# Performance work log

Hardware: AMD Instinct MI355X
Metric: run time of the kernel (lower is better)

## Reference

```python
import jax, jax.numpy as jnp
import numpy as np

N_NODES = 50000


def gcn_conv(x, W, b, src, dst, ew, n):
    """PyG-style GCNConv: D^-1/2 (A+I) D^-1/2 X W + b with self-loops of weight 1."""
    h = x @ W                                   # [N, out]
    loop = jnp.arange(n, dtype=src.dtype)
    s = jnp.concatenate([src, loop])            # [E+N]
    d = jnp.concatenate([dst, loop])
    w = jnp.concatenate([ew, jnp.ones((n,), dtype=x.dtype)])
    deg = jax.ops.segment_sum(w, d, num_segments=n)
    dinv = jnp.where(deg > 0, jax.lax.rsqrt(deg), 0.0)
    norm = dinv[s] * w * dinv[d]                # [E+N]
    out = jax.ops.segment_sum(h[s] * norm[:, None], d, num_segments=n)
    return out + b


def setup_inputs() -> dict:
    key = jax.random.key(0)
    ks = jax.random.split(key, 12)
    in_feats, hidden = 128, 128
    half = hidden // 2
    E = 800000
    x = jax.random.normal(ks[0], (N_NODES, in_feats), dtype=jnp.float32)
    edge_index = jax.random.randint(ks[1], (2, E), 0, N_NODES, dtype=jnp.int64)
    edge_weight = jax.random.uniform(ks[2], (E,), dtype=jnp.float32)
    def lin(k, fan_in, shape):
        bound = 1.0 / np.sqrt(fan_in)
        return jax.random.uniform(k, shape, minval=-bound, maxval=bound, dtype=jnp.float32)
    return {
        "x": x,
        "edge_index": edge_index,
        "edge_weight": edge_weight,
        "W1": lin(ks[3], in_feats, (in_feats, hidden)),
        "b1": jnp.zeros((hidden,), jnp.float32),
        "W2": lin(ks[4], hidden, (hidden, hidden)),
        "b2": jnp.zeros((hidden,), jnp.float32),
        "Ws": lin(ks[5], in_feats, (in_feats, hidden)),
        "bs": lin(ks[6], in_feats, (hidden,)),
        "Wl": lin(ks[7], in_feats, (in_feats, half)),
        "bl": jnp.zeros((half,), jnp.float32),
        "Wl2": lin(ks[8], half, (half, 1)),
        "bl2": lin(ks[9], half, (1,)),
    }


def reference(x, edge_index, edge_weight, W1, b1, W2, b2, Ws, bs, Wl, bl, Wl2, bl2):
    n = x.shape[0]
    src, dst = edge_index[0], edge_index[1]
    # conv1 + ReLU over neighbors
    h_neighbors = jax.nn.relu(gcn_conv(x, W1, b1, src, dst, edge_weight, n))
    # leader score: GCNConv -> ReLU -> Linear(.,1) -> sigmoid, per node
    ls_h = jax.nn.relu(gcn_conv(x, Wl, bl, src, dst, edge_weight, n))
    leader_score = jax.nn.sigmoid(ls_h @ Wl2 + bl2)        # [N, 1]
    # gated fusion of self projection vs neighbor aggregation
    h_self_proj = x @ Ws + bs
    h_new = (1.0 - leader_score) * h_neighbors + leader_score * h_self_proj
    h_final = jax.nn.relu(gcn_conv(h_new, W2, b2, src, dst, edge_weight, n))
    return (h_final, leader_score)
```

## Files before the change

kernel.cpp:

```cpp
#include <hip/hip_runtime.h>
#include <math.h>

#define THREADS 256
#define ELLS 96
#define GEMM_YSTRIDE 104
#define NPHA 256
#define BSHIFT 7
#define NBMAX 392
#define BCAP 4096
#define PMAX 5872
#define LMAX 736

typedef unsigned int uint32;
typedef unsigned long long ull64;
typedef __attribute__((ext_vector_type(8))) short bf16x8;
typedef __attribute__((ext_vector_type(4))) float f32x4;
typedef __attribute__((ext_vector_type(2))) float f32x2;

__device__ __forceinline__ unsigned short f2bf_rne(float x) {
  uint32 u = __float_as_uint(x);
  u += 0x7fffu + ((u >> 16) & 1u);
  return (unsigned short)(u >> 16);
}

__device__ __forceinline__ f32x2 dw2f2(uint32 d) {
  f32x2 r;
  r.x = __uint_as_float(d << 16);
  r.y = __uint_as_float(d & 0xffff0000u);
  return r;
}


__global__ __launch_bounds__(256) void prep_fused(uint32* __restrict__ gcnt, int n,
                                                  const float* __restrict__ W1, const float* __restrict__ Wl,
                                                  const float* __restrict__ Ws, const float* __restrict__ W2,
                                                  unsigned short* __restrict__ whi, unsigned short* __restrict__ wlo,
                                                  const float* __restrict__ x, unsigned short* __restrict__ xraw,
                                                  int nW) {
  int b = blockIdx.x;
  int t = threadIdx.x;
  if (b == 0) {
    for (int k = t; k < NBMAX; k += 256) gcnt[k] = 0u;
  }
  if (b < 1 + nW) {
    if (b == 0) return;
    int idx = (b - 1) * 256 + t;
    if (idx >= 448 * 128) return;
    int slot = idx >> 7;
    int k = idx & 127;
    const float* W; int ncol, ncols;
    if (slot < 128)      { W = W1; ncol = slot;       ncols = 128; }
    else if (slot < 192) { W = Wl; ncol = slot - 128; ncols = 64;  }
    else if (slot < 320) { W = Ws; ncol = slot - 192; ncols = 128; }
    else                 { W = W2; ncol = slot - 320; ncols = 128; }
    float v = W[(size_t)k * ncols + ncol];
    unsigned short hi = f2bf_rne(v);
    float hif = __uint_as_float((uint32)hi << 16);
    unsigned short lo = f2bf_rne(v - hif);
    whi[idx] = hi;
    wlo[idx] = lo;
  } else {
    int i = (b - 1 - nW) * 256 + t;
    if (i >= n * 16) return;
    const float* px = x + (size_t)i * 8;
    float4 a = *(const float4*)px;
    float4 c = *(const float4*)(px + 4);
    ushort4 r0, r1;
    r0.x = f2bf_rne(a.x); r0.y = f2bf_rne(a.y); r0.z = f2bf_rne(a.z); r0.w = f2bf_rne(a.w);
    r1.x = f2bf_rne(c.x); r1.y = f2bf_rne(c.y); r1.z = f2bf_rne(c.z); r1.w = f2bf_rne(c.w);
    *(ushort4*)(xraw + (size_t)i * 8) = r0;
    *(ushort4*)(xraw + (size_t)i * 8 + 4) = r1;
  }
}


struct Chunk {
  const unsigned short* A;
  const unsigned short* whi;
  const unsigned short* wlo;
  const float* bias;
  void* out;
  int ostride;
  int obf16;
};
struct GemmArgs { Chunk c[2]; };

__device__ __forceinline__ void gemm_body(const Chunk& d, int M, int nTiles, int tile0, int tstride) {
  const unsigned short* A = d.A;
  int w = threadIdx.x >> 6, lane = threadIdx.x & 63;
  int n16 = lane & 15, quad = lane >> 4;

  bf16x8 Bh[4][4], Bl[4][4];
  {
    const unsigned short* wh = d.whi + (size_t)n16 * 128 + quad * 8;
    const unsigned short* wl = d.wlo + (size_t)n16 * 128 + quad * 8;
#pragma unroll
    for (int ct = 0; ct < 4; ct++)
#pragma unroll
      for (int ks = 0; ks < 4; ks++) {
        Bh[ct][ks] = *(const bf16x8*)(wh + ct * 16 * 128 + ks * 32);
        Bl[ct][ks] = *(const bf16x8*)(wl + ct * 16 * 128 + ks * 32);
      }
  }
  float bv[4];
#pragma unroll
  for (int ct = 0; ct < 4; ct++) bv[ct] = d.bias ? d.bias[ct * 16 + n16] : 0.f;

  int tile = tile0;
  bf16x8 av0[4], av1[4];
  if (tile < nTiles) {
    int bm = tile * 128;
    int r0 = bm + w * 32 + n16, r1 = r0 + 16;
    int r0c = r0 < M ? r0 : M - 1;
    int r1c = r1 < M ? r1 : M - 1;
    const unsigned short* a0 = A + (size_t)r0c * 128 + quad * 8;
    const unsigned short* a1 = A + (size_t)r1c * 128 + quad * 8;
#pragma unroll
    for (int ks = 0; ks < 4; ks++) {
      av0[ks] = *(const bf16x8*)(a0 + ks * 32);
      av1[ks] = *(const bf16x8*)(a1 + ks * 32);
    }
  }

  for (; tile < nTiles; tile += tstride) {
    int nxt = tile + tstride;
    bf16x8 nv0[4], nv1[4];
    if (nxt < nTiles) {
      int bm = nxt * 128;
      int r0 = bm + w * 32 + n16, r1 = r0 + 16;
      int r0c = r0 < M ? r0 : M - 1;
      int r1c = r1 < M ? r1 : M - 1;
      const unsigned short* a0 = A + (size_t)r0c * 128 + quad * 8;
      const unsigned short* a1 = A + (size_t)r1c * 128 + quad * 8;
#pragma unroll
      for (int ks = 0; ks < 4; ks++) {
        nv0[ks] = *(const bf16x8*)(a0 + ks * 32);
        nv1[ks] = *(const bf16x8*)(a1 + ks * 32);
      }
    }

    f32x4 acc[2][4];
#pragma unroll
    for (int rt = 0; rt < 2; rt++)
#pragma unroll
      for (int ct = 0; ct < 4; ct++) acc[rt][ct] = (f32x4){0.f, 0.f, 0.f, 0.f};

#pragma unroll
    for (int ks = 0; ks < 4; ks++)
#pragma unroll
      for (int ct = 0; ct < 4; ct++) {
        acc[0][ct] = __builtin_amdgcn_mfma_f32_16x16x32_bf16(av0[ks], Bh[ct][ks], acc[0][ct], 0, 0, 0);
        acc[0][ct] = __builtin_amdgcn_mfma_f32_16x16x32_bf16(av0[ks], Bl[ct][ks], acc[0][ct], 0, 0, 0);
        acc[1][ct] = __builtin_amdgcn_mfma_f32_16x16x32_bf16(av1[ks], Bh[ct][ks], acc[1][ct], 0, 0, 0);
        acc[1][ct] = __builtin_amdgcn_mfma_f32_16x16x32_bf16(av1[ks], Bl[ct][ks], acc[1][ct], 0, 0, 0);
      }

    int bm = tile * 128;
#pragma unroll
    for (int ct = 0; ct < 4; ct++) {
      int col = ct * 16 + n16;
#pragma unroll
      for (int rt = 0; rt < 2; rt++) {
#pragma unroll
        for (int reg = 0; reg < 4; reg++) {
          int row = bm + w * 32 + rt * 16 + quad * 4 + reg;
          if (row < M) {
            float v = acc[rt][ct][reg] + bv[ct];
            if (d.obf16)
              ((unsigned short*)d.out)[(size_t)row * d.ostride + col] = f2bf_rne(v);
            else
              ((float*)d.out)[(size_t)row * d.ostride + col] = v;
          }
        }
      }
    }

#pragma unroll
    for (int ks = 0; ks < 4; ks++) { av0[ks] = nv0[ks]; av1[ks] = nv1[ks]; }
  }
}


__global__ __launch_bounds__(256, 2) void fused_sg(GemmArgs args, int M, int nTiles, int nGemm,
                                                   const int* __restrict__ ei, const float* __restrict__ ew,
                                                   uint32* __restrict__ gcnt, uint2* __restrict__ staging, int E) {
  __shared__ uint32 cntS[NBMAX], offS[NBMAX], gbS[NBMAX], curS[NBMAX];
  __shared__ unsigned short lineBk[LMAX];
  __shared__ uint2 sortedS[PMAX];
  __shared__ uint32 Ptot;

  int b = blockIdx.x;
  int gemmIdx = -1, phIdx = -1;
  int twice = nGemm * 2;
  if (b < twice) {
    if (b & 1) gemmIdx = b >> 1; else phIdx = b >> 1;
  } else {
    phIdx = nGemm + (b - twice);
  }

  if (phIdx >= 0) {
    int t = threadIdx.x;
    int per = (E + NPHA - 1) / NPHA;
    int start = phIdx * per;
    int end = start + per; if (end > E) end = E;
    for (int k = t; k < NBMAX; k += 256) cntS[k] = 0u;
    __syncthreads();
    for (int i = start + t; i < end; i += 256)
      atomicAdd(&cntS[(uint32)ei[E + i] >> BSHIFT], 1u);
    __syncthreads();
    if (t < 64) {
      uint32 carry = 0;
      for (int base = 0; base < NBMAX; base += 64) {
        int k = base + t;
        uint32 v = (k < NBMAX) ? ((cntS[k] + 7u) & ~7u) : 0u;
        uint32 s = v;
#pragma unroll
        for (int dd = 1; dd < 64; dd <<= 1) {
          uint32 o = __shfl_up(s, dd);
          if (t >= dd) s += o;
        }
        if (k < NBMAX) offS[k] = carry + s - v;
        carry += __shfl(s, 63);
      }
      if (t == 0) Ptot = carry;
    }
    __syncthreads();
    uint32 P = Ptot;
    for (int k = t; k < NBMAX; k += 256) {
      uint32 pc = (cntS[k] + 7u) & ~7u;
      gbS[k] = pc ? atomicAdd(&gcnt[k], pc) : 0u;
      curS[k] = 0u;
      uint32 l1 = (offS[k] + pc) >> 3;
      for (uint32 l = offS[k] >> 3; l < l1; l++) lineBk[l] = (unsigned short)k;
    }
    for (uint32 j = t; j < P; j += 256) sortedS[j] = make_uint2(0xFFFFFFFFu, 0u);
    __syncthreads();
    for (int i = start + t; i < end; i += 256) {
      int d = ei[E + i];
      int s = ei[i];
      float w = ew[i];
      int bk = d >> BSHIFT;
      uint32 pos = offS[bk] + atomicAdd(&curS[bk], 1u);
      sortedS[pos] = make_uint2(((uint32)(d & 127) << 24) | (uint32)s, __float_as_uint(w));
    }
    __syncthreads();
    for (uint32 j = t; j < P; j += 256) {
      int k = lineBk[j >> 3];
      uint32 idx = gbS[k] + (j - offS[k]);
      if (idx < BCAP)
        staging[(size_t)k * BCAP + idx] = sortedS[j];
    }
    return;
  }

  int chunkId = gemmIdx & 1;
  int ytile = gemmIdx >> 1;
  gemm_body(args.c[chunkId], M, nTiles, ytile, GEMM_YSTRIDE);
}


__global__ __launch_bounds__(256) void phaseB_kernel(const uint2* __restrict__ staging,
                                                     const uint32* __restrict__ gcnt,
                                                     int2* __restrict__ ell,
                                                     float* __restrict__ dinv, int* __restrict__ cnt32, int n) {
  __shared__ uint32 cntL[128], sumL[128];
  int b = blockIdx.x;
  int t = threadIdx.x;
  if (t < 128) { cntL[t] = 0u; sumL[t] = 0u; }
  __syncthreads();
  uint32 cnt = gcnt[b]; if (cnt > BCAP) cnt = BCAP;
  const uint2* sb = staging + (size_t)b * BCAP;
  int dbase = b << BSHIFT;
  for (uint32 i = t; i < cnt; i += 256) {
    uint2 en = sb[i];
    if ((en.x >> 24) == 0xFFu) continue;
    int dl = (int)(en.x >> 24);
    int s = (int)(en.x & 0xffffffu);
    float w = __uint_as_float(en.y);
    uint32 fx = (uint32)(w * 8388608.0f + 0.5f);
    atomicAdd(&sumL[dl], fx);
    uint32 slot = atomicAdd(&cntL[dl], 1u);
    if (slot < ELLS)
      ell[(size_t)(dbase + dl) * ELLS + slot] = make_int2(s, __float_as_int(w));
  }
  __syncthreads();
  if (t < 128) {
    int d = dbase + t;
    if (d < n) {
      const float S = 1.1920928955078125e-7f;
      dinv[d] = rsqrtf(1.0f + (float)sumL[t] * S);
      uint32 c = cntL[t];
      cnt32[d] = (int)(c < ELLS ? c : ELLS);
    }
  }
}


__global__ __launch_bounds__(256) void aggx_kernel(const unsigned short* __restrict__ xr,
                                                   const int* __restrict__ cnt,
                                                   const int2* __restrict__ csr,
                                                   const float* __restrict__ dinv,
                                                   unsigned short* __restrict__ z, int nnodes) {
  int wave = threadIdx.x >> 6;
  int lane = threadIdx.x & 63;
  int node = blockIdx.x * 4 + wave;
  if (node >= nnodes) return;
  int g = lane >> 4, q = lane & 15;
  int rs = node * ELLS;
  int n = cnt[node];
  float di = dinv[node];
  f32x2 dv2 = {di, di};

  f32x2 acc[4] = {};
  if (g == 0) {
    uint4 v = *(const uint4*)(xr + (size_t)node * 128 + 8 * q);
    acc[0] = dv2 * dw2f2(v.x); acc[1] = dv2 * dw2f2(v.y);
    acc[2] = dv2 * dw2f2(v.z); acc[3] = dv2 * dw2f2(v.w);
  }
  int e = g;
  for (; e + 4 < n; e += 8) {
    int2 en0 = csr[rs + e];
    int2 en1 = csr[rs + e + 4];
    float wz0 = __int_as_float(en0.y) * dinv[en0.x];
    float wz1 = __int_as_float(en1.y) * dinv[en1.x];
    f32x2 w0 = {wz0, wz0};
    f32x2 w1 = {wz1, wz1};
    uint4 a0 = *(const uint4*)(xr + (size_t)en0.x * 128 + 8 * q);
    uint4 a1 = *(const uint4*)(xr + (size_t)en1.x * 128 + 8 * q);
    acc[0] += w0 * dw2f2(a0.x) + w1 * dw2f2(a1.x);
    acc[1] += w0 * dw2f2(a0.y) + w1 * dw2f2(a1.y);
    acc[2] += w0 * dw2f2(a0.z) + w1 * dw2f2(a1.z);
    acc[3] += w0 * dw2f2(a0.w) + w1 * dw2f2(a1.w);
  }
  if (e < n) {
    int2 en = csr[rs + e];
    float wz0 = __int_as_float(en.y) * dinv[en.x];
    f32x2 w0 = {wz0, wz0};
    uint4 a0 = *(const uint4*)(xr + (size_t)en.x * 128 + 8 * q);
    acc[0] += w0 * dw2f2(a0.x);
    acc[1] += w0 * dw2f2(a0.y);
    acc[2] += w0 * dw2f2(a0.z);
    acc[3] += w0 * dw2f2(a0.w);
  }
#pragma unroll
  for (int k = 0; k < 4; k++) {
    acc[k].x += __shfl_xor(acc[k].x, 16);
    acc[k].y += __shfl_xor(acc[k].y, 16);
    acc[k].x += __shfl_xor(acc[k].x, 32);
    acc[k].y += __shfl_xor(acc[k].y, 32);
  }
  if (g == 0) {
    float r[8];
    r[0] = di * acc[0].x; r[1] = di * acc[0].y; r[2] = di * acc[1].x; r[3] = di * acc[1].y;
    r[4] = di * acc[2].x; r[5] = di * acc[2].y; r[6] = di * acc[3].x; r[7] = di * acc[3].y;
    ushort4 p0, p1;
    p0.x = f2bf_rne(r[0]); p0.y = f2bf_rne(r[1]); p0.z = f2bf_rne(r[2]); p0.w = f2bf_rne(r[3]);
    p1.x = f2bf_rne(r[4]); p1.y = f2bf_rne(r[5]); p1.z = f2bf_rne(r[6]); p1.w = f2bf_rne(r[7]);
    *(ushort4*)(z + (size_t)node * 128 + 8 * q) = p0;
    *(ushort4*)(z + (size_t)node * 128 + 8 * q + 4) = p1;
  }
}


__global__ __launch_bounds__(256) void gemm_fused(const unsigned short* __restrict__ z,
                                                  const unsigned short* __restrict__ hsp,
                                                  const unsigned short* __restrict__ whi,
                                                  const unsigned short* __restrict__ wlo,
                                                  const float* __restrict__ b1, const float* __restrict__ bl,
                                                  const float* __restrict__ Wl2, const float* __restrict__ bl2,
                                                  const float* __restrict__ dinv,
                                                  unsigned short* __restrict__ h2_out,
                                                  float* __restrict__ leader_out, int n) {
  __shared__ unsigned short hn[128][136];
  int tile = blockIdx.x;
  int w = threadIdx.x >> 6, lane = threadIdx.x & 63;
  int n16 = lane & 15, quad = lane >> 4;
  int bm = tile * 128;

  bf16x8 av[2][4];
#pragma unroll
  for (int rt = 0; rt < 2; rt++) {
    int r = bm + w * 32 + rt * 16 + n16;
    int rc = r < n ? r : n - 1;
    const unsigned short* a = z + (size_t)rc * 128 + quad * 8;
#pragma unroll
    for (int ks = 0; ks < 4; ks++) av[rt][ks] = *(const bf16x8*)(a + ks * 32);
  }

  float lgate[2][4];
  {
    f32x4 ls[2][4];
#pragma unroll
    for (int rt = 0; rt < 2; rt++)
#pragma unroll
      for (int cf = 0; cf < 4; cf++) ls[rt][cf] = (f32x4){0.f, 0.f, 0.f, 0.f};
#pragma unroll
    for (int cf = 0; cf < 4; cf++) {
      const unsigned short* wh = whi + (size_t)(128 + cf * 16 + n16) * 128 + quad * 8;
      const unsigned short* wl = wlo + (size_t)(128 + cf * 16 + n16) * 128 + quad * 8;
#pragma unroll
      for (int ks = 0; ks < 4; ks++) {
        bf16x8 Bh = *(const bf16x8*)(wh + ks * 32);
        bf16x8 Bl = *(const bf16x8*)(wl + ks * 32);
        ls[0][cf] = __builtin_amdgcn_mfma_f32_16x16x32_bf16(av[0][ks], Bh, ls[0][cf], 0, 0, 0);
        ls[0][cf] = __builtin_amdgcn_mfma_f32_16x16x32_bf16(av[0][ks], Bl, ls[0][cf], 0, 0, 0);
        ls[1][cf] = __builtin_amdgcn_mfma_f32_16x16x32_bf16(av[1][ks], Bh, ls[1][cf], 0, 0, 0);
        ls[1][cf] = __builtin_amdgcn_mfma_f32_16x16x32_bf16(av[1][ks], Bl, ls[1][cf], 0, 0, 0);
      }
    }
#pragma unroll
    for (int rt = 0; rt < 2; rt++)
#pragma unroll
      for (int reg = 0; reg < 4; reg++) {
        float p = 0.f;
#pragma unroll
        for (int cf = 0; cf < 4; cf++) {
          int col = cf * 16 + n16;
          p += fmaxf(ls[rt][cf][reg] + bl[col], 0.f) * Wl2[col];
        }
        p += __shfl_xor(p, 1);
        p += __shfl_xor(p, 2);
        p += __shfl_xor(p, 4);
        p += __shfl_xor(p, 8);
        float lv = 1.f / (1.f + expf(-(p + bl2[0])));
        lgate[rt][reg] = lv;
        int row = bm + w * 32 + rt * 16 + quad * 4 + reg;
        if (n16 == 0 && row < n) leader_out[row] = lv;
      }
  }

  float dirr[2][4];
#pragma unroll
  for (int rt = 0; rt < 2; rt++)
#pragma unroll
    for (int reg = 0; reg < 4; reg++) {
      int row = bm + w * 32 + rt * 16 + quad * 4 + reg;
      dirr[rt][reg] = row < n ? dinv[row] : 0.f;
    }

#pragma unroll
  for (int cf = 0; cf < 8; cf++) {
    f32x4 h0 = {0.f, 0.f, 0.f, 0.f}, h1v = {0.f, 0.f, 0.f, 0.f};
    const unsigned short* wh = whi + (size_t)(cf * 16 + n16) * 128 + quad * 8;
    const unsigned short* wl = wlo + (size_t)(cf * 16 + n16) * 128 + quad * 8;
#pragma unroll
    for (int ks = 0; ks < 4; ks++) {
      bf16x8 Bh = *(const bf16x8*)(wh + ks * 32);
      bf16x8 Bl = *(const bf16x8*)(wl + ks * 32);
      h0 = __builtin_amdgcn_mfma_f32_16x16x32_bf16(av[0][ks], Bh, h0, 0, 0, 0);
      h0 = __builtin_amdgcn_mfma_f32_16x16x32_bf16(av[0][ks], Bl, h0, 0, 0, 0);
      h1v = __builtin_amdgcn_mfma_f32_16x16x32_bf16(av[1][ks], Bh, h1v, 0, 0, 0);
      h1v = __builtin_amdgcn_mfma_f32_16x16x32_bf16(av[1][ks], Bl, h1v, 0, 0, 0);
    }
    int col = cf * 16 + n16;
    float bc = b1[col];
#pragma unroll
    for (int rt = 0; rt < 2; rt++) {
      f32x4 a = rt ? h1v : h0;
#pragma unroll
      for (int reg = 0; reg < 4; reg++) {
        int row = bm + w * 32 + rt * 16 + quad * 4 + reg;
        int rc = row < n ? row : n - 1;
        float hs = __uint_as_float((uint32)hsp[(size_t)rc * 128 + col] << 16);
        float rl = fmaxf(a[reg] + bc, 0.f);
        float lv = lgate[rt][reg];
        float hv = ((1.f - lv) * rl + lv * hs) * dirr[rt][reg];
        hn[w * 32 + rt * 16 + quad * 4 + reg][col] = f2bf_rne(hv);
      }
    }
  }
  __syncthreads();

  bf16x8 av2[2][4];
#pragma unroll
  for (int rt = 0; rt < 2; rt++)
#pragma unroll
    for (int ks = 0; ks < 4; ks++)
      av2[rt][ks] = *(const bf16x8*)&hn[w * 32 + rt * 16 + n16][quad * 8 + ks * 32];
#pragma unroll
  for (int cf = 0; cf < 8; cf++) {
    f32x4 h0 = {0.f, 0.f, 0.f, 0.f}, h1v = {0.f, 0.f, 0.f, 0.f};
    const unsigned short* wh = whi + (size_t)(320 + cf * 16 + n16) * 128 + quad * 8;
    const unsigned short* wl = wlo + (size_t)(320 + cf * 16 + n16) * 128 + quad * 8;
#pragma unroll
    for (int ks = 0; ks < 4; ks++) {
      bf16x8 Bh = *(const bf16x8*)(wh + ks * 32);
      bf16x8 Bl = *(const bf16x8*)(wl + ks * 32);
      h0 = __builtin_amdgcn_mfma_f32_16x16x32_bf16(av2[0][ks], Bh, h0, 0, 0, 0);
      h0 = __builtin_amdgcn_mfma_f32_16x16x32_bf16(av2[0][ks], Bl, h0, 0, 0, 0);
      h1v = __builtin_amdgcn_mfma_f32_16x16x32_bf16(av2[1][ks], Bh, h1v, 0, 0, 0);
      h1v = __builtin_amdgcn_mfma_f32_16x16x32_bf16(av2[1][ks], Bl, h1v, 0, 0, 0);
    }
    int col = cf * 16 + n16;
#pragma unroll
    for (int rt = 0; rt < 2; rt++) {
      f32x4 a = rt ? h1v : h0;
#pragma unroll
      for (int reg = 0; reg < 4; reg++) {
        int row = bm + w * 32 + rt * 16 + quad * 4 + reg;
        if (row < n) h2_out[(size_t)row * 128 + col] = f2bf_rne(a[reg]);
      }
    }
  }
}


__global__ __launch_bounds__(256) void agg_conv2_kernel(const unsigned short* __restrict__ h,
                                                        const int* __restrict__ cnt,
                                                        const int2* __restrict__ csr,
                                                        const float* __restrict__ dinv, const float* __restrict__ bias,
                                                        float* __restrict__ out, int nnodes) {
  int wave = threadIdx.x >> 6;
  int lane = threadIdx.x & 63;
  int node = blockIdx.x * 4 + wave;
  if (node >= nnodes) return;
  int g = lane >> 4;
  int q = lane & 15;
  int rs = node * ELLS;
  int n = cnt[node];
  float di = dinv[node];

  f32x2 acc[4] = {};
  if (g == 0) {
    uint4 v = *(const uint4*)(h + (size_t)node * 128 + 8 * q);
    acc[0] = dw2f2(v.x); acc[1] = dw2f2(v.y);
    acc[2] = dw2f2(v.z); acc[3] = dw2f2(v.w);
  }
  int e = g;
  for (; e + 4 < n; e += 8) {
    int2 en0 = csr[rs + e];
    int2 en1 = csr[rs + e + 4];
    f32x2 w0 = {__int_as_float(en0.y), __int_as_float(en0.y)};
    f32x2 w1 = {__int_as_float(en1.y), __int_as_float(en1.y)};
    uint4 v0 = *(const uint4*)(h + (size_t)en0.x * 128 + 8 * q);
    uint4 v1 = *(const uint4*)(h + (size_t)en1.x * 128 + 8 * q);
    acc[0] += w0 * dw2f2(v0.x) + w1 * dw2f2(v1.x);
    acc[1] += w0 * dw2f2(v0.y) + w1 * dw2f2(v1.y);
    acc[2] += w0 * dw2f2(v0.z) + w1 * dw2f2(v1.z);
    acc[3] += w0 * dw2f2(v0.w) + w1 * dw2f2(v1.w);
  }
  if (e < n) {
    int2 en = csr[rs + e];
    f32x2 w0 = {__int_as_float(en.y), __int_as_float(en.y)};
    uint4 v = *(const uint4*)(h + (size_t)en.x * 128 + 8 * q);
    acc[0] += w0 * dw2f2(v.x);
    acc[1] += w0 * dw2f2(v.y);
    acc[2] += w0 * dw2f2(v.z);
    acc[3] += w0 * dw2f2(v.w);
  }
#pragma unroll
  for (int k = 0; k < 4; k++) {
    acc[k].x += __shfl_xor(acc[k].x, 16);
    acc[k].y += __shfl_xor(acc[k].y, 16);
    acc[k].x += __shfl_xor(acc[k].x, 32);
    acc[k].y += __shfl_xor(acc[k].y, 32);
  }
  if (g == 0) {
    float b[8], r[8];
    *(float4*)&b[0] = *(const float4*)(bias + 8 * q);
    *(float4*)&b[4] = *(const float4*)(bias + 8 * q + 4);
    float a[8];
    a[0] = acc[0].x; a[1] = acc[0].y; a[2] = acc[1].x; a[3] = acc[1].y;
    a[4] = acc[2].x; a[5] = acc[2].y; a[6] = acc[3].x; a[7] = acc[3].y;
#pragma unroll
    for (int j = 0; j < 8; j++) r[j] = fmaxf(di * a[j] + b[j], 0.f);
    *(float4*)(out + (size_t)node * 128 + 8 * q) = *(float4*)&r[0];
    *(float4*)(out + (size_t)node * 128 + 8 * q + 4) = *(float4*)&r[4];
  }
}


extern "C" void kernel_launch(void* const* d_in, const int* in_sizes, int n_in,
                              void* d_out, int out_size, void* d_ws, size_t ws_size,
                              hipStream_t stream) {
  const float* x   = (const float*)d_in[0];
  const int*   ei  = (const int*)d_in[1];
  const float* ew  = (const float*)d_in[2];
  const float* W1  = (const float*)d_in[3];
  const float* b1  = (const float*)d_in[4];
  const float* W2  = (const float*)d_in[5];
  const float* b2  = (const float*)d_in[6];
  const float* Wsp = (const float*)d_in[7];
  const float* bs  = (const float*)d_in[8];
  const float* Wl  = (const float*)d_in[9];
  const float* bl  = (const float*)d_in[10];
  const float* Wl2 = (const float*)d_in[11];
  const float* bl2 = (const float*)d_in[12];

  const int N = in_sizes[0] / 128;
  const int E = in_sizes[1] / 2;
  const int NB = (N + 127) >> BSHIFT;

  char* ws = (char*)d_ws;
  size_t off = 0;
  auto alloc = [&](size_t bytes) -> void* {
    void* p = ws + off;
    off = (off + bytes + 255) & ~(size_t)255;
    return p;
  };
  uint32* gcnt     = (uint32*)alloc((size_t)NBMAX * 4);
  uint2* staging   = (uint2*)alloc((size_t)NBMAX * BCAP * 8);
  float* dinv      = (float*)alloc((size_t)N * 4);
  int*   cnt32     = (int*)alloc((size_t)N * 4);
  int2*  ell       = (int2*)alloc((size_t)N * ELLS * 8);
  unsigned short* xraw  = (unsigned short*)alloc((size_t)N * 128 * 2);
  unsigned short* zbf   = (unsigned short*)alloc((size_t)N * 128 * 2);
  unsigned short* h2bf  = (unsigned short*)alloc((size_t)N * 128 * 2);
  unsigned short* hspbf = (unsigned short*)alloc((size_t)N * 128 * 2);
  unsigned short* whi = (unsigned short*)alloc((size_t)448 * 128 * 2);
  unsigned short* wlo = (unsigned short*)alloc((size_t)448 * 128 * 2);

  float* h_final = (float*)d_out;
  float* leader  = (float*)d_out + (size_t)N * 128;

  int gWave = (N + 3) / 4;
  int nTiles = (N + 127) / 128;
  int nCast = (N * 16 + 255) / 256;
  int nW = (448 * 128 + 255) / 256;

  prep_fused<<<1 + nW + nCast, 256, 0, stream>>>(gcnt, N, W1, Wl, Wsp, W2, whi, wlo, x, xraw, nW);

  {
    GemmArgs ga;
    ga.c[0] = {xraw, whi + 192 * 128, wlo + 192 * 128, bs,      hspbf,      128, 1};
    ga.c[1] = {xraw, whi + 256 * 128, wlo + 256 * 128, bs + 64, hspbf + 64, 128, 1};
    int nGemm = 2 * GEMM_YSTRIDE;
    int totalBlocks = NPHA + nGemm;
    fused_sg<<<totalBlocks, 256, 0, stream>>>(ga, N, nTiles, nGemm, ei, ew, gcnt, staging, E);
  }

  phaseB_kernel<<<NB, 256, 0, stream>>>(staging, gcnt, ell, dinv, cnt32, N);

  aggx_kernel<<<gWave, 256, 0, stream>>>(xraw, cnt32, ell, dinv, zbf, N);

  gemm_fused<<<nTiles, 256, 0, stream>>>(zbf, hspbf, whi, wlo, b1, bl, Wl2, bl2,
                                         dinv, h2bf, leader, N);

  agg_conv2_kernel<<<gWave, 256, 0, stream>>>(h2bf, cnt32, ell,
                                              dinv, b2, h_final, N);
}
```

Before: 252.3 us.

## Shrink fused GEMM tile to 16 rows per wave, drop block barrier

The fused conv1/leader/conv2-transform GEMM kernel now gives each wave 16 rows instead of 32 and launches twice as many blocks (64 rows per block). Each wave keeps a private LDS slice, so the __syncthreads between the two GEMM stages goes away. The self-projection values are also preloaded up front. This aims to raise occupancy and parallelism across the GPU's CUs, at the cost of every wave loading the weight B fragments for half as many rows, which doubles weight traffic per row.

```diff
diff --git a/kernel.cpp b/kernel.cpp
--- a/kernel.cpp
+++ b/kernel.cpp
@@ -371,29 +371,38 @@
                                                   const float* __restrict__ dinv,
                                                   unsigned short* __restrict__ h2_out,
                                                   float* __restrict__ leader_out, int n) {
-  __shared__ unsigned short hn[128][136];
-  int tile = blockIdx.x;
-  int w = threadIdx.x >> 6, lane = threadIdx.x & 63;
+  __shared__ unsigned short hn[4][16][136];
+  int wave = threadIdx.x >> 6, lane = threadIdx.x & 63;
   int n16 = lane & 15, quad = lane >> 4;
-  int bm = tile * 128;
-
-  bf16x8 av[2][4];
-#pragma unroll
-  for (int rt = 0; rt < 2; rt++) {
-    int r = bm + w * 32 + rt * 16 + n16;
+  int base = blockIdx.x * 64 + wave * 16;
+  if (base >= n) return;
+
+  bf16x8 av[4];
+  {
+    int r = base + n16;
     int rc = r < n ? r : n - 1;
     const unsigned short* a = z + (size_t)rc * 128 + quad * 8;
 #pragma unroll
-    for (int ks = 0; ks < 4; ks++) av[rt][ks] = *(const bf16x8*)(a + ks * 32);
-  }
-
-  float lgate[2][4];
+    for (int ks = 0; ks < 4; ks++) av[ks] = *(const bf16x8*)(a + ks * 32);
+  }
+
+  float dirr[4];
+  unsigned short hsv[8][4];
+#pragma unroll
+  for (int reg = 0; reg < 4; reg++) {
+    int row = base + quad * 4 + reg;
+    dirr[reg] = row < n ? dinv[row] : 0.f;
+    int rc = row < n ? row : n - 1;
+#pragma unroll
+    for (int cf = 0; cf < 8; cf++)
+      hsv[cf][reg] = hsp[(size_t)rc * 128 + cf * 16 + n16];
+  }
+
+  float lgate[4];
   {
-    f32x4 ls[2][4];
-#pragma unroll
-    for (int rt = 0; rt < 2; rt++)
-#pragma unroll
-      for (int cf = 0; cf < 4; cf++) ls[rt][cf] = (f32x4){0.f, 0.f, 0.f, 0.f};
+    f32x4 ls[4];
+#pragma unroll
+    for (int cf = 0; cf < 4; cf++) ls[cf] = (f32x4){0.f, 0.f, 0.f, 0.f};
 #pragma unroll
     for (int cf = 0; cf < 4; cf++) {
       const unsigned short* wh = whi + (size_t)(128 + cf * 16 + n16) * 128 + quad * 8;
@@ -402,104 +411,74 @@
       for (int ks = 0; ks < 4; ks++) {
         bf16x8 Bh = *(const bf16x8*)(wh + ks * 32);
         bf16x8 Bl = *(const bf16x8*)(wl + ks * 32);
-        ls[0][cf] = __builtin_amdgcn_mfma_f32_16x16x32_bf16(av[0][ks], Bh, ls[0][cf], 0, 0, 0);
-        ls[0][cf] = __builtin_amdgcn_mfma_f32_16x16x32_bf16(av[0][ks], Bl, ls[0][cf], 0, 0, 0);
-        ls[1][cf] = __builtin_amdgcn_mfma_f32_16x16x32_bf16(av[1][ks], Bh, ls[1][cf], 0, 0, 0);
-        ls[1][cf] = __builtin_amdgcn_mfma_f32_16x16x32_bf16(av[1][ks], Bl, ls[1][cf], 0, 0, 0);
+        ls[cf] = __builtin_amdgcn_mfma_f32_16x16x32_bf16(av[ks], Bh, ls[cf], 0, 0, 0);
+        ls[cf] = __builtin_amdgcn_mfma_f32_16x16x32_bf16(av[ks], Bl, ls[cf], 0, 0, 0);
       }
     }
 #pragma unroll
-    for (int rt = 0; rt < 2; rt++)
-#pragma unroll
-      for (int reg = 0; reg < 4; reg++) {
-        float p = 0.f;
-#pragma unroll
-        for (int cf = 0; cf < 4; cf++) {
-          int col = cf * 16 + n16;
-          p += fmaxf(ls[rt][cf][reg] + bl[col], 0.f) * Wl2[col];
-        }
-        p += __shfl_xor(p, 1);
-        p += __shfl_xor(p, 2);
-        p += __shfl_xor(p, 4);
-        p += __shfl_xor(p, 8);
-        float lv = 1.f / (1.f + expf(-(p + bl2[0])));
-        lgate[rt][reg] = lv;
-        int row = bm + w * 32 + rt * 16 + quad * 4 + reg;
-        if (n16 == 0 && row < n) leader_out[row] = lv;
+    for (int reg = 0; reg < 4; reg++) {
+      float p = 0.f;
+#pragma unroll
+      for (int cf = 0; cf < 4; cf++) {
+        int col = cf * 16 + n16;
+        p += fmaxf(ls[cf][reg] + bl[col], 0.f) * Wl2[col];
       }
-  }
-
-  float dirr[2][4];
-#pragma unroll
-  for (int rt = 0; rt < 2; rt++)
-#pragma unroll
-    for (int reg = 0; reg < 4; reg++) {
-      int row = bm + w * 32 + rt * 16 + quad * 4 + reg;
-      dirr[rt][reg] = row < n ? dinv[row] : 0.f;
-    }
+      p += __shfl_xor(p, 1);
+      p += __shfl_xor(p, 2);
+      p += __shfl_xor(p, 4);
+      p += __shfl_xor(p, 8);
+      float lv = 1.f / (1.f + expf(-(p + bl2[0])));
+      lgate[reg] = lv;
+      int row = base + quad * 4 + reg;
+      if (n16 == 0 && row < n) leader_out[row] = lv;
+    }
+  }
 
 #pragma unroll
   for (int cf = 0; cf < 8; cf++) {
-    f32x4 h0 = {0.f, 0.f, 0.f, 0.f}, h1v = {0.f, 0.f, 0.f, 0.f};
+    f32x4 h0 = {0.f, 0.f, 0.f, 0.f};
     const unsigned short* wh = whi + (size_t)(cf * 16 + n16) * 128 + quad * 8;
     const unsigned short* wl = wlo + (size_t)(cf * 16 + n16) * 128 + quad * 8;
 #pragma unroll
     for (int ks = 0; ks < 4; ks++) {
       bf16x8 Bh = *(const bf16x8*)(wh + ks * 32);
       bf16x8 Bl = *(const bf16x8*)(wl + ks * 32);
-      h0 = __builtin_amdgcn_mfma_f32_16x16x32_bf16(av[0][ks], Bh, h0, 0, 0, 0);
-      h0 = __builtin_amdgcn_mfma_f32_16x16x32_bf16(av[0][ks], Bl, h0, 0, 0, 0);
-      h1v = __builtin_amdgcn_mfma_f32_16x16x32_bf16(av[1][ks], Bh, h1v, 0, 0, 0);
-      h1v = __builtin_amdgcn_mfma_f32_16x16x32_bf16(av[1][ks], Bl, h1v, 0, 0, 0);
+      h0 = __builtin_amdgcn_mfma_f32_16x16x32_bf16(av[ks], Bh, h0, 0, 0, 0);
+      h0 = __builtin_amdgcn_mfma_f32_16x16x32_bf16(av[ks], Bl, h0, 0, 0, 0);
     }
     int col = cf * 16 + n16;
     float bc = b1[col];
 #pragma unroll
-    for (int rt = 0; rt < 2; rt++) {
-      f32x4 a = rt ? h1v : h0;
-#pragma unroll
-      for (int reg = 0; reg < 4; reg++) {
-        int row = bm + w * 32 + rt * 16 + quad * 4 + reg;
-        int rc = row < n ? row : n - 1;
-        float hs = __uint_as_float((uint32)hsp[(size_t)rc * 128 + col] << 16);
-        float rl = fmaxf(a[reg] + bc, 0.f);
-        float lv = lgate[rt][reg];
-        float hv = ((1.f - lv) * rl + lv * hs) * dirr[rt][reg];
-        hn[w * 32 + rt * 16 + quad * 4 + reg][col] = f2bf_rne(hv);
-      }
-    }
-  }
-  __syncthreads();
-
-  bf16x8 av2[2][4];
-#pragma unroll
-  for (int rt = 0; rt < 2; rt++)
-#pragma unroll
-    for (int ks = 0; ks < 4; ks++)
-      av2[rt][ks] = *(const bf16x8*)&hn[w * 32 + rt * 16 + n16][quad * 8 + ks * 32];
+    for (int reg = 0; reg < 4; reg++) {
+      float hs = __uint_as_float((uint32)hsv[cf][reg] << 16);
+      float rl = fmaxf(h0[reg] + bc, 0.f);
+      float lv = lgate[reg];
+      float hv = ((1.f - lv) * rl + lv * hs) * dirr[reg];
+      hn[wave][quad * 4 + reg][col] = f2bf_rne(hv);
+    }
+  }
+
+  bf16x8 av2[4];
+#pragma unroll
+  for (int ks = 0; ks < 4; ks++)
+    av2[ks] = *(const bf16x8*)&hn[wave][n16][quad * 8 + ks * 32];
 #pragma unroll
   for (int cf = 0; cf < 8; cf++) {
-    f32x4 h0 = {0.f, 0.f, 0.f, 0.f}, h1v = {0.f, 0.f, 0.f, 0.f};
+    f32x4 h0 = {0.f, 0.f, 0.f, 0.f};
     const unsigned short* wh = whi + (size_t)(320 + cf * 16 + n16) * 128 + quad * 8;
     const unsigned short* wl = wlo + (size_t)(320 + cf * 16 + n16) * 128 + quad * 8;
 #pragma unroll
     for (int ks = 0; ks < 4; ks++) {
       bf16x8 Bh = *(const bf16x8*)(wh + ks * 32);
       bf16x8 Bl = *(const bf16x8*)(wl + ks * 32);
-      h0 = __builtin_amdgcn_mfma_f32_16x16x32_bf16(av2[0][ks], Bh, h0, 0, 0, 0);
-      h0 = __builtin_amdgcn_mfma_f32_16x16x32_bf16(av2[0][ks], Bl, h0, 0, 0, 0);
-      h1v = __builtin_amdgcn_mfma_f32_16x16x32_bf16(av2[1][ks], Bh, h1v, 0, 0, 0);
-      h1v = __builtin_amdgcn_mfma_f32_16x16x32_bf16(av2[1][ks], Bl, h1v, 0, 0, 0);
+      h0 = __builtin_amdgcn_mfma_f32_16x16x32_bf16(av2[ks], Bh, h0, 0, 0, 0);
+      h0 = __builtin_amdgcn_mfma_f32_16x16x32_bf16(av2[ks], Bl, h0, 0, 0, 0);
     }
     int col = cf * 16 + n16;
 #pragma unroll
-    for (int rt = 0; rt < 2; rt++) {
-      f32x4 a = rt ? h1v : h0;
-#pragma unroll
-      for (int reg = 0; reg < 4; reg++) {
-        int row = bm + w * 32 + rt * 16 + quad * 4 + reg;
-        if (row < n) h2_out[(size_t)row * 128 + col] = f2bf_rne(a[reg]);
-      }
+    for (int reg = 0; reg < 4; reg++) {
+      int row = base + quad * 4 + reg;
+      if (row < n) h2_out[(size_t)row * 128 + col] = f2bf_rne(h0[reg]);
     }
   }
 }
@@ -617,6 +596,7 @@
   int nTiles = (N + 127) / 128;
   int nCast = (N * 16 + 255) / 256;
   int nW = (448 * 128 + 255) / 256;
+  int gFuse = (N + 63) / 64;
 
   prep_fused<<<1 + nW + nCast, 256, 0, stream>>>(gcnt, N, W1, Wl, Wsp, W2, whi, wlo, x, xraw, nW);
 
@@ -633,8 +613,8 @@
 
   aggx_kernel<<<gWave, 256, 0, stream>>>(xraw, cnt32, ell, dinv, zbf, N);
 
-  gemm_fused<<<nTiles, 256, 0, stream>>>(zbf, hspbf, whi, wlo, b1, bl, Wl2, bl2,
-                                         dinv, h2bf, leader, N);
+  gemm_fused<<<gFuse, 256, 0, stream>>>(zbf, hspbf, whi, wlo, b1, bl, Wl2, bl2,
+                                        dinv, h2bf, leader, N);
 
   agg_conv2_kernel<<<gWave, 256, 0, stream>>>(h2bf, cnt32, ell,
                                               dinv, b2, h_final, N);
```

Result: slower. 278.7 us (+10.5%).

## Make fused GEMM single-wave per block with prefetched weight fragments

Applied to the files above, without the earlier changes.

Turns the fused GEMM into one 64-thread wave per block over 32 rows, so the __syncthreads barrier goes away and the grid holds more, smaller blocks. The hsp self-projection values and dinv are loaded up front, and weight B-fragments are double-buffered across column tiles so global loads overlap with MFMAs. The trade-off is higher register pressure from the prefetched fragments and the hsv array, which could lower occupancy or cause spills.

```diff
diff --git a/kernel.cpp b/kernel.cpp
--- a/kernel.cpp
+++ b/kernel.cpp
@@ -362,30 +362,44 @@
 }
 
 
-__global__ __launch_bounds__(256) void gemm_fused(const unsigned short* __restrict__ z,
-                                                  const unsigned short* __restrict__ hsp,
-                                                  const unsigned short* __restrict__ whi,
-                                                  const unsigned short* __restrict__ wlo,
-                                                  const float* __restrict__ b1, const float* __restrict__ bl,
-                                                  const float* __restrict__ Wl2, const float* __restrict__ bl2,
-                                                  const float* __restrict__ dinv,
-                                                  unsigned short* __restrict__ h2_out,
-                                                  float* __restrict__ leader_out, int n) {
-  __shared__ unsigned short hn[128][136];
-  int tile = blockIdx.x;
-  int w = threadIdx.x >> 6, lane = threadIdx.x & 63;
+__global__ __launch_bounds__(64) void gemm_fused(const unsigned short* __restrict__ z,
+                                                 const unsigned short* __restrict__ hsp,
+                                                 const unsigned short* __restrict__ whi,
+                                                 const unsigned short* __restrict__ wlo,
+                                                 const float* __restrict__ b1, const float* __restrict__ bl,
+                                                 const float* __restrict__ Wl2, const float* __restrict__ bl2,
+                                                 const float* __restrict__ dinv,
+                                                 unsigned short* __restrict__ h2_out,
+                                                 float* __restrict__ leader_out, int n) {
+  __shared__ unsigned short hn[32][136];
+  int lane = threadIdx.x;
   int n16 = lane & 15, quad = lane >> 4;
-  int bm = tile * 128;
+  int bm = blockIdx.x * 32;
+  if (bm >= n) return;
 
   bf16x8 av[2][4];
 #pragma unroll
   for (int rt = 0; rt < 2; rt++) {
-    int r = bm + w * 32 + rt * 16 + n16;
+    int r = bm + rt * 16 + n16;
     int rc = r < n ? r : n - 1;
     const unsigned short* a = z + (size_t)rc * 128 + quad * 8;
 #pragma unroll
     for (int ks = 0; ks < 4; ks++) av[rt][ks] = *(const bf16x8*)(a + ks * 32);
   }
+
+  float dirr[2][4];
+  unsigned short hsv[2][8][4];
+#pragma unroll
+  for (int rt = 0; rt < 2; rt++)
+#pragma unroll
+    for (int reg = 0; reg < 4; reg++) {
+      int row = bm + rt * 16 + quad * 4 + reg;
+      dirr[rt][reg] = row < n ? dinv[row] : 0.f;
+      int rc = row < n ? row : n - 1;
+#pragma unroll
+      for (int cf = 0; cf < 8; cf++)
+        hsv[rt][cf][reg] = hsp[(size_t)rc * 128 + cf * 16 + n16];
+    }
 
   float lgate[2][4];
   {
@@ -394,18 +408,28 @@
     for (int rt = 0; rt < 2; rt++)
 #pragma unroll
       for (int cf = 0; cf < 4; cf++) ls[rt][cf] = (f32x4){0.f, 0.f, 0.f, 0.f};
+    bf16x8 Bh[2][4], Bl[2][4];
+#pragma unroll
+    for (int ks = 0; ks < 4; ks++) {
+      Bh[0][ks] = *(const bf16x8*)(whi + (size_t)(128 + n16) * 128 + quad * 8 + ks * 32);
+      Bl[0][ks] = *(const bf16x8*)(wlo + (size_t)(128 + n16) * 128 + quad * 8 + ks * 32);
+    }
 #pragma unroll
     for (int cf = 0; cf < 4; cf++) {
-      const unsigned short* wh = whi + (size_t)(128 + cf * 16 + n16) * 128 + quad * 8;
-      const unsigned short* wl = wlo + (size_t)(128 + cf * 16 + n16) * 128 + quad * 8;
+      int cur = cf & 1, nxt = cur ^ 1;
+      if (cf < 3) {
+#pragma unroll
+        for (int ks = 0; ks < 4; ks++) {
+          Bh[nxt][ks] = *(const bf16x8*)(whi + (size_t)(128 + (cf + 1) * 16 + n16) * 128 + quad * 8 + ks * 32);
+          Bl[nxt][ks] = *(const bf16x8*)(wlo + (size_t)(128 + (cf + 1) * 16 + n16) * 128 + quad * 8 + ks * 32);
+        }
+      }
 #pragma unroll
       for (int ks = 0; ks < 4; ks++) {
-        bf16x8 Bh = *(const bf16x8*)(wh + ks * 32);
-        bf16x8 Bl = *(const bf16x8*)(wl + ks * 32);
-        ls[0][cf] = __builtin_amdgcn_mfma_f32_16x16x32_bf16(av[0][ks], Bh, ls[0][cf], 0, 0, 0);
-        ls[0][cf] = __builtin_amdgcn_mfma_f32_16x16x32_bf16(av[0][ks], Bl, ls[0][cf], 0, 0, 0);
-        ls[1][cf] = __builtin_amdgcn_mfma_f32_16x16x32_bf16(av[1][ks], Bh, ls[1][cf], 0, 0, 0);
-        ls[1][cf] = __builtin_amdgcn_mfma_f32_16x16x32_bf16(av[1][ks], Bl, ls[1][cf], 0, 0, 0);
+        ls[0][cf] = __builtin_amdgcn_mfma_f32_16x16x32_bf16(av[0][ks], Bh[cur][ks], ls[0][cf], 0, 0, 0);
+        ls[0][cf] = __builtin_amdgcn_mfma_f32_16x16x32_bf16(av[0][ks], Bl[cur][ks], ls[0][cf], 0, 0, 0);
+        ls[1][cf] = __builtin_amdgcn_mfma_f32_16x16x32_bf16(av[1][ks], Bh[cur][ks], ls[1][cf], 0, 0, 0);
+        ls[1][cf] = __builtin_amdgcn_mfma_f32_16x16x32_bf16(av[1][ks], Bl[cur][ks], ls[1][cf], 0, 0, 0);
       }
     }
 #pragma unroll
@@ -424,81 +448,93 @@
         p += __shfl_xor(p, 8);
         float lv = 1.f / (1.f + expf(-(p + bl2[0])));
         lgate[rt][reg] = lv;
-        int row = bm + w * 32 + rt * 16 + quad * 4 + reg;
+        int row = bm + rt * 16 + quad * 4 + reg;
         if (n16 == 0 && row < n) leader_out[row] = lv;
       }
   }
 
-  float dirr[2][4];
+  {
+    bf16x8 Bh[2][4], Bl[2][4];
+#pragma unroll
+    for (int ks = 0; ks < 4; ks++) {
+      Bh[0][ks] = *(const bf16x8*)(whi + (size_t)n16 * 128 + quad * 8 + ks * 32);
+      Bl[0][ks] = *(const bf16x8*)(wlo + (size_t)n16 * 128 + quad * 8 + ks * 32);
+    }
+#pragma unroll
+    for (int cf = 0; cf < 8; cf++) {
+      int cur = cf & 1, nxt = cur ^ 1;
+      if (cf < 7) {
+#pragma unroll
+        for (int ks = 0; ks < 4; ks++) {
+          Bh[nxt][ks] = *(const bf16x8*)(whi + (size_t)((cf + 1) * 16 + n16) * 128 + quad * 8 + ks * 32);
+          Bl[nxt][ks] = *(const bf16x8*)(wlo + (size_t)((cf + 1) * 16 + n16) * 128 + quad * 8 + ks * 32);
+        }
+      }
+      f32x4 h0 = {0.f, 0.f, 0.f, 0.f}, h1v = {0.f, 0.f, 0.f, 0.f};
+#pragma unroll
+      for (int ks = 0; ks < 4; ks++) {
+        h0 = __builtin_amdgcn_mfma_f32_16x16x32_bf16(av[0][ks], Bh[cur][ks], h0, 0, 0, 0);
+        h0 = __builtin_amdgcn_mfma_f32_16x16x32_bf16(av[0][ks], Bl[cur][ks], h0, 0, 0, 0);
+        h1v = __builtin_amdgcn_mfma_f32_16x16x32_bf16(av[1][ks], Bh[cur][ks], h1v, 0, 0, 0);
+        h1v = __builtin_amdgcn_mfma_f32_16x16x32_bf16(av[1][ks], Bl[cur][ks], h1v, 0, 0, 0);
+      }
+      int col = cf * 16 + n16;
+      float bc = b1[col];
+#pragma unroll
+      for (int rt = 0; rt < 2; rt++) {
+        f32x4 a = rt ? h1v : h0;
+#pragma unroll
+        for (int reg = 0; reg < 4; reg++) {
+          float hs = __uint_as_float((uint32)hsv[rt][cf][reg] << 16);
+          float rl = fmaxf(a[reg] + bc, 0.f);
+          float lv = lgate[rt][reg];
+          float hv = ((1.f - lv) * rl + lv * hs) * dirr[rt][reg];
+          hn[rt * 16 + quad * 4 + reg][col] = f2bf_rne(hv);
+        }
+      }
+    }
+  }
+
+  bf16x8 av2[2][4];
 #pragma unroll
   for (int rt = 0; rt < 2; rt++)
 #pragma unroll
-    for (int reg = 0; reg < 4; reg++) {
-      int row = bm + w * 32 + rt * 16 + quad * 4 + reg;
-      dirr[rt][reg] = row < n ? dinv[row] : 0.f;
-    }
-
-#pragma unroll
-  for (int cf = 0; cf < 8; cf++) {
-    f32x4 h0 = {0.f, 0.f, 0.f, 0.f}, h1v = {0.f, 0.f, 0.f, 0.f};
-    const unsigned short* wh = whi + (size_t)(cf * 16 + n16) * 128 + quad * 8;
-    const unsigned short* wl = wlo + (size_t)(cf * 16 + n16) * 128 + quad * 8;
+    for (int ks = 0; ks < 4; ks++)
+      av2[rt][ks] = *(const bf16x8*)&hn[rt * 16 + n16][quad * 8 + ks * 32];
+  {
+    bf16x8 Bh[2][4], Bl[2][4];
 #pragma unroll
     for (int ks = 0; ks < 4; ks++) {
-      bf16x8 Bh = *(const bf16x8*)(wh + ks * 32);
-      bf16x8 Bl = *(const bf16x8*)(wl + ks * 32);
-      h0 = __builtin_amdgcn_mfma_f32_16x16x32_bf16(av[0][ks], Bh, h0, 0, 0, 0);
-      h0 = __builtin_amdgcn_mfma_f32_16x16x32_bf16(av[0][ks], Bl, h0, 0, 0, 0);
-      h1v = __builtin_amdgcn_mfma_f32_16x16x32_bf16(av[1][ks], Bh, h1v, 0, 0, 0);
-      h1v = __builtin_amdgcn_mfma_f32_16x16x32_bf16(av[1][ks], Bl, h1v, 0, 0, 0);
-    }
-    int col = cf * 16 + n16;
-    float bc = b1[col];
-#pragma unroll
-    for (int rt = 0; rt < 2; rt++) {
-      f32x4 a = rt ? h1v : h0;
-#pragma unroll
-      for (int reg = 0; reg < 4; reg++) {
-        int row = bm + w * 32 + rt * 16 + quad * 4 + reg;
-        int rc = row < n ? row : n - 1;
-        float hs = __uint_as_float((uint32)hsp[(size_t)rc * 128 + col] << 16);
-        float rl = fmaxf(a[reg] + bc, 0.f);
-        float lv = lgate[rt][reg];
-        float hv = ((1.f - lv) * rl + lv * hs) * dirr[rt][reg];
-        hn[w * 32 + rt * 16 + quad * 4 + reg][col] = f2bf_rne(hv);
-      }
-    }
-  }
-  __syncthreads();
-
-  bf16x8 av2[2][4];
-#pragma unroll
-  for (int rt = 0; rt < 2; rt++)
-#pragma unroll
-    for (int ks = 0; ks < 4; ks++)
-      av2[rt][ks] = *(const bf16x8*)&hn[w * 32 + rt * 16 + n16][quad * 8 + ks * 32];
-#pragma unroll
-  for (int cf = 0; cf < 8; cf++) {
-    f32x4 h0 = {0.f, 0.f, 0.f, 0.f}, h1v = {0.f, 0.f, 0.f, 0.f};
-    const unsigned short* wh = whi + (size_t)(320 + cf * 16 + n16) * 128 + quad * 8;
-    const unsigned short* wl = wlo + (size_t)(320 + cf * 16 + n16) * 128 + quad * 8;
-#pragma unroll
-    for (int ks = 0; ks < 4; ks++) {
-      bf16x8 Bh = *(const bf16x8*)(wh + ks * 32);
-      bf16x8 Bl = *(const bf16x8*)(wl + ks * 32);
-      h0 = __builtin_amdgcn_mfma_f32_16x16x32_bf16(av2[0][ks], Bh, h0, 0, 0, 0);
-      h0 = __builtin_amdgcn_mfma_f32_16x16x32_bf16(av2[0][ks], Bl, h0, 0, 0, 0);
-      h1v = __builtin_amdgcn_mfma_f32_16x16x32_bf16(av2[1][ks], Bh, h1v, 0, 0, 0);
-      h1v = __builtin_amdgcn_mfma_f32_16x16x32_bf16(av2[1][ks], Bl, h1v, 0, 0, 0);
-    }
-    int col = cf * 16 + n16;
-#pragma unroll
-    for (int rt = 0; rt < 2; rt++) {
-      f32x4 a = rt ? h1v : h0;
-#pragma unroll
-      for (int reg = 0; reg < 4; reg++) {
-        int row = bm + w * 32 + rt * 16 + quad * 4 + reg;
-        if (row < n) h2_out[(size_t)row * 128 + col] = f2bf_rne(a[reg]);
+      Bh[0][ks] = *(const bf16x8*)(whi + (size_t)(320 + n16) * 128 + quad * 8 + ks * 32);
+      Bl[0][ks] = *(const bf16x8*)(wlo + (size_t)(320 + n16) * 128 + quad * 8 + ks * 32);
+    }
+#pragma unroll
+    for (int cf = 0; cf < 8; cf++) {
+      int cur = cf & 1, nxt = cur ^ 1;
+      if (cf < 7) {
+#pragma unroll
+        for (int ks = 0; ks < 4; ks++) {
+          Bh[nxt][ks] = *(const bf16x8*)(whi + (size_t)(320 + (cf + 1) * 16 + n16) * 128 + quad * 8 + ks * 32);
+          Bl[nxt][ks] = *(const bf16x8*)(wlo + (size_t)(320 + (cf + 1) * 16 + n16) * 128 + quad * 8 + ks * 32);
+        }
+      }
+      f32x4 h0 = {0.f, 0.f, 0.f, 0.f}, h1v = {0.f, 0.f, 0.f, 0.f};
+#pragma unroll
+      for (int ks = 0; ks < 4; ks++) {
+        h0 = __builtin_amdgcn_mfma_f32_16x16x32_bf16(av2[0][ks], Bh[cur][ks], h0, 0, 0, 0);
+        h0 = __builtin_amdgcn_mfma_f32_16x16x32_bf16(av2[0][ks], Bl[cur][ks], h0, 0, 0, 0);
+        h1v = __builtin_amdgcn_mfma_f32_16x16x32_bf16(av2[1][ks], Bh[cur][ks], h1v, 0, 0, 0);
+        h1v = __builtin_amdgcn_mfma_f32_16x16x32_bf16(av2[1][ks], Bl[cur][ks], h1v, 0, 0, 0);
+      }
+      int col = cf * 16 + n16;
+#pragma unroll
+      for (int rt = 0; rt < 2; rt++) {
+        f32x4 a = rt ? h1v : h0;
+#pragma unroll
+        for (int reg = 0; reg < 4; reg++) {
+          int row = bm + rt * 16 + quad * 4 + reg;
+          if (row < n) h2_out[(size_t)row * 128 + col] = f2bf_rne(a[reg]);
+        }
       }
     }
   }
@@ -617,6 +653,7 @@
   int nTiles = (N + 127) / 128;
   int nCast = (N * 16 + 255) / 256;
   int nW = (448 * 128 + 255) / 256;
+  int gFuse = (N + 31) / 32;
 
   prep_fused<<<1 + nW + nCast, 256, 0, stream>>>(gcnt, N, W1, Wl, Wsp, W2, whi, wlo, x, xraw, nW);
 
@@ -633,8 +670,8 @@
 
   aggx_kernel<<<gWave, 256, 0, stream>>>(xraw, cnt32, ell, dinv, zbf, N);
 
-  gemm_fused<<<nTiles, 256, 0, stream>>>(zbf, hspbf, whi, wlo, b1, bl, Wl2, bl2,
-                                         dinv, h2bf, leader, N);
+  gemm_fused<<<gFuse, 64, 0, stream>>>(zbf, hspbf, whi, wlo, b1, bl, Wl2, bl2,
+                                       dinv, h2bf, leader, N);
 
   agg_conv2_kernel<<<gWave, 256, 0, stream>>>(h2bf, cnt32, ell,
                                               dinv, b2, h_final, N);
```

New measurement: 244.3 us. 3.2% less time.
